# Kernel optimization log

Measured on AMD Instinct MI355X. Metric: run time of the kernel, lower is better.

The kernel has to match this reference:

```python
import jax, jax.numpy as jnp
import numpy as np

NB, NL, V, VOCAB, D, TOPK = 16, 64, 16384, 32000, 256, 16
NITER, EARLY, RW = 8, 2, 0.8


def setup_inputs():
    key = jax.random.key(0)
    ks = jax.random.split(key, 8)
    probas = jax.random.uniform(ks[0], (NB, NL, V), dtype=jnp.float32) + 1e-6
    h_d = jax.random.normal(ks[1], (NB, NL, D), dtype=jnp.float32)
    lengths = jax.random.randint(ks[2], (NB,), NL // 2, NL + 1)
    mask = (jnp.arange(NL)[None, :] < lengths[:, None]).astype(jnp.int32)  # prefix mask
    batch_vocab = jax.random.randint(ks[3], (V,), 0, VOCAB)
    emb_table = jax.random.normal(ks[4], (VOCAB, D), dtype=jnp.float32) * 0.02
    W1 = jax.random.normal(ks[5], (2 * D, D), dtype=jnp.float32) * 0.006
    b1 = jnp.zeros((D,), dtype=jnp.float32)
    return {"probas": probas, "h_d": h_d, "mask": mask, "batch_vocab": batch_vocab,
            "emb_table": emb_table, "W1": W1, "b1": b1}


def _forward(probas, h_d, mask, batch_vocab, emb_table, W1, b1):
    maskf = mask.astype(probas.dtype)
    MAP = jnp.argmax(probas, axis=-1)                       # [nb,nl]
    topk_vals, topk_idx = jax.lax.top_k(probas, TOPK)       # [nb,nl,K]
    topk_vals = jnp.where(mask[..., None] < 1, 1.0, topk_vals)
    logits = jnp.log(topk_vals)                             # Categorical(probs) == categorical(log p)
    sLens = jnp.sum(mask, axis=1)                           # [nb]
    one_hot = jnp.arange(NL)[None, :] == (sLens - 1)[:, None]  # one_hot_by_mask: last valid pos
    m2d = (mask[:, :, None] * mask[:, None, :]) > 0
    eyeM = jnp.eye(NL, dtype=probas.dtype)
    h_masked = h_d * maskf[..., None]

    def step(carry, k):
        max_score, best, count, stopped = carry
        choice = jax.random.categorical(k, logits)          # [nb,nl]
        samples = jnp.take_along_axis(topk_idx, choice[..., None], axis=-1)[..., 0]
        samples = jnp.where(one_hot, MAP, samples)
        embs = emb_table[batch_vocab[samples]] * maskf[..., None]   # gather+embed, masked
        new_embs = jax.nn.relu(jnp.concatenate([embs, h_masked], axis=-1) @ W1 + b1)
        Kmat = jnp.einsum('bld,bmd->blm', new_embs, new_embs)       # [nb,nl,nl]
        # det of leading lxl submatrix == det with padded rows/cols replaced by identity
        score = jnp.linalg.det(jnp.where(m2d, Kmat, eyeM))          # [nb]
        improved = score > max_score
        any_imp = jnp.any(improved)
        count = jnp.where(any_imp, 0, count + 1)
        upd = improved & (~stopped)
        stopped = stopped | ((~any_imp) & (count >= EARLY))
        max_score = jnp.where(upd, score, max_score)
        best = jnp.where(upd[:, None], samples, best)
        return (max_score, best, count, stopped), None

    init = (jnp.full((NB,), -jnp.inf, probas.dtype), MAP, jnp.int32(0), jnp.bool_(False))
    keys = jax.random.split(jax.random.key(42), NITER)
    (max_score, best, _, _), _ = jax.lax.scan(step, init, keys)

    # diverse_proba: scatter redist_weight at best choice, (1-rw) elsewhere, renormalize
    am = jnp.where(jnp.arange(V)[None, None, :] == best[:, :, None], RW, 1.0 - RW).astype(probas.dtype)
    x = probas * am
    nm = jnp.sum(x, axis=-1, keepdims=True)
    nm = jnp.where(maskf[..., None] == 0, 1e-10, nm)
    return x / nm, max_score


def reference(probas, h_d, mask, batch_vocab, emb_table, W1, b1):
    return _forward(probas, h_d, mask, batch_vocab, emb_table, W1, b1)
```

## Files before the change

kernel.cpp:

```cpp
#include <hip/hip_runtime.h>
#include <math.h>
#include <stdint.h>


#define TINYF 1.17549435082228750797e-38f

#define KMX(r, c) (((r) * 68) + ((c) ^ ((((r) >> 3) & 7) << 2)))

struct Keys16 { uint32_t k[16]; };

__host__ __device__ inline void tf2x32(uint32_t k0, uint32_t k1,
                                       uint32_t x0, uint32_t x1,
                                       uint32_t* o0, uint32_t* o1) {
  uint32_t ks2 = k0 ^ k1 ^ 0x1BD11BDAu;
  uint32_t ks[3] = {k0, k1, ks2};
  uint32_t v0 = x0 + k0, v1 = x1 + k1;
  const int R0[4] = {13, 15, 26, 6};
  const int R1[4] = {17, 29, 16, 24};
#pragma unroll
  for (int g = 0; g < 5; ++g) {
    const int* RR = (g & 1) ? R1 : R0;
#pragma unroll
    for (int r = 0; r < 4; ++r) {
      v0 += v1;
      v1 = (v1 << RR[r]) | (v1 >> (32 - RR[r]));
      v1 ^= v0;
    }
    v0 += ks[(g + 1) % 3];
    v1 += ks[(g + 2) % 3] + (uint32_t)(g + 1);
  }
  *o0 = v0; *o1 = v1;
}

__device__ inline float logf_ref(float x) { return (float)log((double)x); }

__device__ inline unsigned long long u64max(unsigned long long a,
                                            unsigned long long b) {
  return (a > b) ? a : b;
}

__device__ inline float lane_bcast_f32(float v, int slane) {
  return __uint_as_float(
      (unsigned)__builtin_amdgcn_readlane(__float_as_int(v), slane));
}

__global__ __launch_bounds__(256) void k_topk(const float* __restrict__ probas,
                                              const int* __restrict__ mask,
                                              int* __restrict__ topk_idx,
                                              float* __restrict__ logits,
                                              float* __restrict__ S) {
  int row = blockIdx.x;
  int t = threadIdx.x;
  const float* p = probas + (size_t)row * 16384;
  __shared__ unsigned long long lists[256][16];
  __shared__ float swsum[4];
  __shared__ int lcnt;
  unsigned long long* cand = &lists[0][0];

  cand[t] = 0ull;
  cand[t + 256] = 0ull;
  if (t == 0) lcnt = 0;
  __syncthreads();

  const uint32_t TB = 0x3F7E0000u;
  float sum = 0.f;
  const float4* p4 = (const float4*)p;
#pragma unroll 4
  for (int j = 0; j < 16; ++j) {
    float4 x = p4[t + j * 256];
    int v0 = (t + j * 256) * 4;
    uint32_t u0 = __float_as_uint(x.x), u1 = __float_as_uint(x.y);
    uint32_t u2 = __float_as_uint(x.z), u3 = __float_as_uint(x.w);
    sum += x.x; sum += x.y; sum += x.z; sum += x.w;
    uint32_t um = max(max(u0, u1), max(u2, u3));
    if (um >= TB) {
      if (u0 >= TB) { int s = atomicAdd(&lcnt, 1); if (s < 512)
          cand[s] = ((unsigned long long)u0 << 32) | (unsigned)(~(v0 + 0)); }
      if (u1 >= TB) { int s = atomicAdd(&lcnt, 1); if (s < 512)
          cand[s] = ((unsigned long long)u1 << 32) | (unsigned)(~(v0 + 1)); }
      if (u2 >= TB) { int s = atomicAdd(&lcnt, 1); if (s < 512)
          cand[s] = ((unsigned long long)u2 << 32) | (unsigned)(~(v0 + 2)); }
      if (u3 >= TB) { int s = atomicAdd(&lcnt, 1); if (s < 512)
          cand[s] = ((unsigned long long)u3 << 32) | (unsigned)(~(v0 + 3)); }
    }
  }
#pragma unroll
  for (int off = 32; off >= 1; off >>= 1) sum += __shfl_down(sum, off);
  if ((t & 63) == 0) swsum[t >> 6] = sum;
  __syncthreads();
  if (t == 0) S[row] = ((swsum[0] + swsum[1]) + swsum[2]) + swsum[3];

  int n = lcnt;
  if (n >= 16 && n <= 512) {
    if (t < 64) {
      unsigned long long c[8];
#pragma unroll
      for (int k = 0; k < 8; ++k) c[k] = cand[t + 64 * k];
      unsigned long long win = 0ull;
#pragma unroll
      for (int r = 0; r < 16; ++r) {
        unsigned long long m = c[0];
#pragma unroll
        for (int k = 1; k < 8; ++k) m = u64max(m, c[k]);
#pragma unroll
        for (int off = 32; off >= 1; off >>= 1) {
          unsigned long long o = __shfl_xor(m, off);
          m = u64max(m, o);
        }
        if (t == r) win = m;
#pragma unroll
        for (int k = 0; k < 8; ++k) if (c[k] == m) c[k] = 0ull;
      }
      if (t < 16) {
        int idx = (int)(~(unsigned)(win & 0xFFFFFFFFull));
        float val = __uint_as_float((unsigned)(win >> 32));
        topk_idx[row * 16 + t] = idx;
        logits[row * 16 + t] = (mask[row] == 0) ? 0.0f : logf_ref(val);
      }
    }
    return;
  }

  {
    unsigned long long loc[16];
#pragma unroll
    for (int q = 0; q < 16; ++q) loc[q] = 0ull;
    for (int j = 0; j < 64; ++j) {
      int v = t + j * 256;
      float x = p[v];
      unsigned long long key =
          ((unsigned long long)__float_as_uint(x) << 32) | (unsigned)(~v);
      if (key > loc[15]) {
        loc[15] = key;
#pragma unroll
        for (int q = 15; q > 0; --q) {
          if (loc[q] > loc[q - 1]) {
            unsigned long long tmp = loc[q]; loc[q] = loc[q - 1]; loc[q - 1] = tmp;
          }
        }
      }
    }
    __syncthreads();
#pragma unroll
    for (int q = 0; q < 16; ++q) lists[t][q] = loc[q];
    __syncthreads();
    for (int nl = 128; nl >= 1; nl >>= 1) {
      if (t < nl) {
        unsigned long long M[16];
        int ia = 0, ib = 0;
#pragma unroll
        for (int q = 0; q < 16; ++q) {
          unsigned long long av = lists[t][ia];
          unsigned long long bv = lists[t + nl][ib];
          if (av >= bv) { M[q] = av; ia++; } else { M[q] = bv; ib++; }
        }
#pragma unroll
        for (int q = 0; q < 16; ++q) lists[t][q] = M[q];
      }
      __syncthreads();
    }
    if (t < 16) {
      unsigned long long key = lists[0][t];
      int idx = (int)(~(unsigned)(key & 0xFFFFFFFFull));
      float val = __uint_as_float((unsigned)(key >> 32));
      topk_idx[row * 16 + t] = idx;
      logits[row * 16 + t] = (mask[row] == 0) ? 0.0f : logf_ref(val);
    }
  }
}

__global__ __launch_bounds__(256) void k_sample(Keys16 keys,
                                                const int* __restrict__ mask,
                                                const int* __restrict__ topk_idx,
                                                const float* __restrict__ logits,
                                                int* __restrict__ samples,
                                                int* __restrict__ choice) {
  int tid = blockIdx.x * 256 + threadIdx.x;
  int i = tid >> 10;
  int rbl = tid & 1023;
  int b = rbl >> 6;
  int l = rbl & 63;
  uint32_t k0 = keys.k[2 * i], k1 = keys.k[2 * i + 1];
  int sl = 0;
  for (int m = 0; m < 64; ++m) sl += mask[b * 64 + m];
  float bestv = 0.f; int bestk = 0;
#pragma unroll
  for (int k = 0; k < 16; ++k) {
    uint32_t j = (uint32_t)((b * 64 + l) * 16 + k);
    uint32_t y0, y1;
    tf2x32(k0, k1, 0u, j, &y0, &y1);
    uint32_t bits = y0 ^ y1;
    float f = __uint_as_float((bits >> 9) | 0x3f800000u) - 1.0f;
    float u = fmaxf(TINYF, f * 1.0f + TINYF);
    float t1 = logf_ref(u);
    float g = -logf_ref(-t1);
    float sv = g + logits[rbl * 16 + k];
    if (k == 0 || sv > bestv) { bestv = sv; bestk = k; }
  }
  int ce = (l == sl - 1) ? 0 : bestk;
  choice[tid] = ce;
  samples[tid] = topk_idx[rbl * 16 + ce];
}

__global__ __launch_bounds__(256) void k_ce(const int* __restrict__ topk_idx,
                                            const int* __restrict__ batch_vocab,
                                            const float* __restrict__ emb,
                                            const float* __restrict__ W1,
                                            const float* __restrict__ h_d,
                                            const float* __restrict__ b1,
                                            const int* __restrict__ mask,
                                            const int* __restrict__ choice,
                                            float* __restrict__ Eall) {
  int row = blockIdx.x;
  int t = threadIdx.x;
  __shared__ int smb;
  __shared__ int rid[8];
  __shared__ float e[8][256];
  __shared__ float hl[256];
  if (t == 0) smb = 0;
  float mkf = (float)mask[row];
  hl[t] = h_d[(size_t)row * 256 + t] * mkf;
  __syncthreads();
  if (t < 8) atomicOr(&smb, 1 << choice[t * 1024 + row]);
  __syncthreads();
  int mb = smb;
  if (t < 8) {
    int cnt = __popc(mb);
    int ss = (t < cnt) ? t : 0;
    int kk = 0;
    for (int bit = 0; bit < 16; ++bit) {
      if ((mb >> bit) & 1) {
        if (ss == 0) { kk = bit; break; }
        ss--;
      }
    }
    rid[t] = batch_vocab[topk_idx[row * 16 + kk]];
  }
  __syncthreads();
#pragma unroll
  for (int k = 0; k < 8; ++k) e[k][t] = emb[(size_t)rid[k] * 256 + t];
  __syncthreads();
  float acch = 0.f;
  for (int j0 = 0; j0 < 256; j0 += 4) {
    float4 hv = *(const float4*)&hl[j0];
    float w0 = W1[(256 + j0 + 0) * 256 + t];
    float w1 = W1[(256 + j0 + 1) * 256 + t];
    float w2 = W1[(256 + j0 + 2) * 256 + t];
    float w3 = W1[(256 + j0 + 3) * 256 + t];
    acch = fmaf(hv.x, w0, acch);
    acch = fmaf(hv.y, w1, acch);
    acch = fmaf(hv.z, w2, acch);
    acch = fmaf(hv.w, w3, acch);
  }
  float acc[8];
#pragma unroll
  for (int k = 0; k < 8; ++k) acc[k] = 0.f;
  for (int j0 = 0; j0 < 256; j0 += 4) {
    float w0 = W1[(j0 + 0) * 256 + t];
    float w1 = W1[(j0 + 1) * 256 + t];
    float w2 = W1[(j0 + 2) * 256 + t];
    float w3 = W1[(j0 + 3) * 256 + t];
#pragma unroll
    for (int k = 0; k < 8; ++k) {
      float4 ev = *(const float4*)&e[k][j0];
      acc[k] = fmaf(ev.x, w0, acc[k]);
      acc[k] = fmaf(ev.y, w1, acc[k]);
      acc[k] = fmaf(ev.z, w2, acc[k]);
      acc[k] = fmaf(ev.w, w3, acc[k]);
    }
  }
  float b1v = b1[t];
#pragma unroll
  for (int k = 0; k < 8; ++k) {
    float val = fmaf(mkf, acc[k], acch) + b1v;
    Eall[((size_t)row * 8 + k) * 256 + t] = fmaxf(val, 0.0f);
  }
}

__global__ __launch_bounds__(256, 1) void k_gram(const float* __restrict__ Eall,
                                                 const int* __restrict__ mask,
                                                 const int* __restrict__ choice,
                                                 float* __restrict__ scores) {
  int blk = blockIdx.x;
  int i = blk >> 4, b = blk & 15;
  int t = threadIdx.x;
  __shared__ __align__(16) float Ett[64][68];
  __shared__ __align__(16) float KmF[64 * 68];
  __shared__ int ch[64];
  int mskv = 0;
  if (t < 64) {
    int rowi = b * 64 + t;
    int ml = 0;
#pragma unroll
    for (int ii = 0; ii < 8; ++ii) ml |= 1 << choice[ii * 1024 + rowi];
    int cc = choice[i * 1024 + rowi];
    ch[t] = __popc(ml & ((1 << cc) - 1));
    mskv = mask[rowi];
  }
  __syncthreads();
  int l = t & 63, wd = t >> 6;
  const float* eptr =
      Eall + ((size_t)((b * 64 + l) * 8 + ch[l])) * 256 + wd * 16;
  float acc[16];
#pragma unroll
  for (int q = 0; q < 16; ++q) acc[q] = 0.f;
  int tx = t & 15, ty = t >> 4;
  for (int dt = 0; dt < 4; ++dt) {
    const float* src = eptr + dt * 64;
    float4 v0 = *(const float4*)(src + 0);
    float4 v1 = *(const float4*)(src + 4);
    float4 v2 = *(const float4*)(src + 8);
    float4 v3 = *(const float4*)(src + 12);
    int d0 = wd * 16;
    Ett[d0 +  0][l] = v0.x; Ett[d0 +  1][l] = v0.y;
    Ett[d0 +  2][l] = v0.z; Ett[d0 +  3][l] = v0.w;
    Ett[d0 +  4][l] = v1.x; Ett[d0 +  5][l] = v1.y;
    Ett[d0 +  6][l] = v1.z; Ett[d0 +  7][l] = v1.w;
    Ett[d0 +  8][l] = v2.x; Ett[d0 +  9][l] = v2.y;
    Ett[d0 + 10][l] = v2.z; Ett[d0 + 11][l] = v2.w;
    Ett[d0 + 12][l] = v3.x; Ett[d0 + 13][l] = v3.y;
    Ett[d0 + 14][l] = v3.z; Ett[d0 + 15][l] = v3.w;
    __syncthreads();
#pragma unroll 4
    for (int dd = 0; dd < 64; ++dd) {
      float4 av4 = *(const float4*)&Ett[dd][tx * 4];
      float4 bv4 = *(const float4*)&Ett[dd][ty * 4];
      float avv[4] = {av4.x, av4.y, av4.z, av4.w};
      float bvv[4] = {bv4.x, bv4.y, bv4.z, bv4.w};
#pragma unroll
      for (int a2 = 0; a2 < 4; ++a2)
#pragma unroll
        for (int c2 = 0; c2 < 4; ++c2)
          acc[a2 * 4 + c2] = fmaf(avv[a2], bvv[c2], acc[a2 * 4 + c2]);
    }
    __syncthreads();
  }
#pragma unroll
  for (int a2 = 0; a2 < 4; ++a2)
#pragma unroll
    for (int c2 = 0; c2 < 4; ++c2)
      KmF[KMX(tx * 4 + a2, ty * 4 + c2)] = acc[a2 * 4 + c2];
  __syncthreads();
  if (t >= 64) return;

  unsigned long long bal = __ballot(mskv != 0);
  int L = __popcll(bal);

#define KM_DECL(i) float4 r##i = *(const float4*)&KmF[KMX(t, 4 * i)];
  KM_DECL(0)  KM_DECL(1)  KM_DECL(2)  KM_DECL(3)
  KM_DECL(4)  KM_DECL(5)  KM_DECL(6)  KM_DECL(7)
  KM_DECL(8)  KM_DECL(9)  KM_DECL(10) KM_DECL(11)
  KM_DECL(12) KM_DECL(13) KM_DECL(14) KM_DECL(15)
#undef KM_DECL

  float sdet = 1.f, ssign = 1.f;
  int pos = t;
  float curcol = r0.x;

#pragma unroll 1
  for (int p = 0; p < L; ++p) {
    bool cnd = (pos >= p) && (pos < L);
    unsigned lo = (((unsigned)(63 - pos)) << 6) | (unsigned)t;
    unsigned long long key =
        cnd ? ((((unsigned long long)__float_as_uint(fabsf(curcol))) << 32) | lo)
            : 0ull;
#pragma unroll
    for (int off = 32; off >= 1; off >>= 1) {
      unsigned long long o = __shfl_xor(key, off);
      if (o > key) key = o;
    }
    int lane_rb = (int)(key & 63u);
    int pb = 63 - (int)((key >> 6) & 63u);
    int srb = __builtin_amdgcn_readfirstlane(lane_rb);
    float kpp = lane_bcast_f32(curcol, srb);
    sdet *= kpp;
    if (pb != p) ssign = -ssign;
    int np = pos;
    if (pos == p) np = pb;
    if (t == lane_rb) np = p;
    pos = np;
    bool active = (pos > p) && (pos < L);
    float f = (active && kpp != 0.f) ? (curcol / kpp) : 0.f;
    float nf = -f;
    int pp1 = p + 1;
#define KM_ELIM(i)                                                        \
    if (4 * i + 3 >= pp1) {                                               \
      float px = lane_bcast_f32(r##i.x, srb);                             \
      float py = lane_bcast_f32(r##i.y, srb);                             \
      float pz = lane_bcast_f32(r##i.z, srb);                             \
      float pw = lane_bcast_f32(r##i.w, srb);                             \
      r##i.x = fmaf(nf, px, r##i.x);                                      \
      r##i.y = fmaf(nf, py, r##i.y);                                      \
      r##i.z = fmaf(nf, pz, r##i.z);                                      \
      r##i.w = fmaf(nf, pw, r##i.w);                                      \
      if ((pp1 >> 2) == i) {    \
        int sel = pp1 & 3;                                                \
        curcol = (sel == 0) ? r##i.x : (sel == 1) ? r##i.y                \
               : (sel == 2) ? r##i.z : r##i.w;                            \
      }                                                                   \
    }
    KM_ELIM(0)  KM_ELIM(1)  KM_ELIM(2)  KM_ELIM(3)
    KM_ELIM(4)  KM_ELIM(5)  KM_ELIM(6)  KM_ELIM(7)
    KM_ELIM(8)  KM_ELIM(9)  KM_ELIM(10) KM_ELIM(11)
    KM_ELIM(12) KM_ELIM(13) KM_ELIM(14) KM_ELIM(15)
#undef KM_ELIM
  }
  if (t == 0) scores[i * 16 + b] = sdet * ssign;
}

__global__ __launch_bounds__(256) void k_out(const float* __restrict__ probas,
                                             const int* __restrict__ mask,
                                             const int* __restrict__ samples,
                                             const int* __restrict__ topk_idx,
                                             const float* __restrict__ scores,
                                             const float* __restrict__ S,
                                             float* __restrict__ out,
                                             float* __restrict__ out_ms) {
  int row = blockIdx.x;
  int b = row >> 6;
  int t = threadIdx.x;
  __shared__ float ssc[128];
  if (t < 128) ssc[t] = scores[t];
  __syncthreads();
  float ms[16]; int w[16];
#pragma unroll
  for (int q = 0; q < 16; ++q) { ms[q] = -INFINITY; w[q] = -1; }
  int count = 0; bool stopped = false;
#pragma unroll
  for (int i = 0; i < 8; ++i) {
    bool any = false; bool imp[16];
#pragma unroll
    for (int q = 0; q < 16; ++q) {
      imp[q] = ssc[i * 16 + q] > ms[q];
      any = any || imp[q];
    }
    count = any ? 0 : (count + 1);
#pragma unroll
    for (int q = 0; q < 16; ++q) {
      if (imp[q] && !stopped) { ms[q] = ssc[i * 16 + q]; w[q] = i; }
    }
    stopped = stopped || ((!any) && (count >= 2));
  }
  if (row == 0 && t == 0) {
#pragma unroll
    for (int q = 0; q < 16; ++q) out_ms[q] = ms[q];
  }
  int wi = -1;
#pragma unroll
  for (int q = 0; q < 16; ++q) if (b == q) wi = w[q];

  int best = (wi >= 0) ? samples[wi * 1024 + row] : topk_idx[row * 16];
  const float* p = probas + (size_t)row * 16384;
  float* o = out + (size_t)row * 16384;
  float nm;
  if (mask[row] == 0) {
    nm = 1e-10f;
  } else {
    nm = 0.2f * S[row] + 0.6f * p[best];
  }
  const float4* p4 = (const float4*)p;
  float4* o4 = (float4*)o;
  for (int f = t; f < 4096; f += 256) {
    float4 x = p4[f];
    int v0 = f << 2;
    float4 r;
    r.x = x.x * ((v0 + 0 == best) ? 0.8f : 0.2f) / nm;
    r.y = x.y * ((v0 + 1 == best) ? 0.8f : 0.2f) / nm;
    r.z = x.z * ((v0 + 2 == best) ? 0.8f : 0.2f) / nm;
    r.w = x.w * ((v0 + 3 == best) ? 0.8f : 0.2f) / nm;
    o4[f] = r;
  }
}

extern "C" void kernel_launch(void* const* d_in, const int* in_sizes, int n_in,
                              void* d_out, int out_size, void* d_ws, size_t ws_size,
                              hipStream_t stream) {
  const float* probas = (const float*)d_in[0];
  const float* h_d    = (const float*)d_in[1];
  const int*   mask   = (const int*)d_in[2];
  const int*   bvoc   = (const int*)d_in[3];
  const float* emb    = (const float*)d_in[4];
  const float* W1     = (const float*)d_in[5];
  const float* b1     = (const float*)d_in[6];
  float* out = (float*)d_out;

  char* w = (char*)d_ws;
  int*   topk_idx = (int*)w;   w += 16384 * sizeof(int);
  float* logits   = (float*)w; w += 16384 * sizeof(float);
  float* S        = (float*)w; w += 1024 * sizeof(float);
  int*   samples  = (int*)w;   w += 8192 * sizeof(int);
  int*   choice   = (int*)w;   w += 8192 * sizeof(int);
  float* scores   = (float*)w; w += 128 * sizeof(float);

  float* Eall = out;

  Keys16 keys;
  for (uint32_t i = 0; i < 8; ++i) {
    uint32_t a, bq;
    tf2x32(0u, 42u, 0u, i, &a, &bq);
    keys.k[2 * i] = a; keys.k[2 * i + 1] = bq;
  }

  k_topk<<<1024, 256, 0, stream>>>(probas, mask, topk_idx, logits, S);
  k_sample<<<32, 256, 0, stream>>>(keys, mask, topk_idx, logits, samples, choice);
  k_ce<<<1024, 256, 0, stream>>>(topk_idx, bvoc, emb, W1, h_d, b1, mask, choice,
                                 Eall);
  k_gram<<<128, 256, 0, stream>>>(Eall, mask, choice, scores);
  k_out<<<1024, 256, 0, stream>>>(probas, mask, samples, topk_idx, scores, S,
                                  out, out + 16777216);
}
```

Measured before the change: 281.7 us.

## Pipeline pivot search one column ahead and use DPP max reduction

Replaces the shuffle-based 64-bit argmax butterfly in the determinant's partial-pivoting loop with a DPP row/bcast reduction, reading the result from lane 63. It also computes the next column's eliminated values first, so the pivot search for step p+1 runs before the full row elimination of step p. This takes the cross-lane reduction off the critical dependency chain. The cost is extra register state and more complex bookkeeping for the lookahead column.

```diff
diff --git a/kernel.cpp b/kernel.cpp
--- a/kernel.cpp
+++ b/kernel.cpp
@@ -42,6 +42,26 @@
 __device__ inline float lane_bcast_f32(float v, int slane) {
   return __uint_as_float(
       (unsigned)__builtin_amdgcn_readlane(__float_as_int(v), slane));
+}
+
+template <int CTRL, int RMASK>
+__device__ inline void dpp_max_step(unsigned& hi, unsigned& lo) {
+  unsigned nh = (unsigned)__builtin_amdgcn_update_dpp(
+      0, (int)hi, CTRL, RMASK, 0xF, false);
+  unsigned nl = (unsigned)__builtin_amdgcn_update_dpp(
+      0, (int)lo, CTRL, RMASK, 0xF, false);
+  bool take = (nh > hi) || (nh == hi && nl > lo);
+  hi = take ? nh : hi;
+  lo = take ? nl : lo;
+}
+
+__device__ inline void dpp_reduce_max64(unsigned& hi, unsigned& lo) {
+  dpp_max_step<0x111, 0xF>(hi, lo);
+  dpp_max_step<0x112, 0xF>(hi, lo);
+  dpp_max_step<0x114, 0xF>(hi, lo);
+  dpp_max_step<0x118, 0xF>(hi, lo);
+  dpp_max_step<0x142, 0xA>(hi, lo);
+  dpp_max_step<0x143, 0xC>(hi, lo);
 }
 
 __global__ __launch_bounds__(256) void k_topk(const float* __restrict__ probas,
@@ -356,33 +376,41 @@
   float sdet = 1.f, ssign = 1.f;
   int pos = t;
   float curcol = r0.x;
+  float nextcol = r0.y;
+
+  unsigned khi, klo;
+  {
+    bool cnd = (pos < L);
+    khi = cnd ? __float_as_uint(fabsf(curcol)) : 0u;
+    klo = cnd ? ((((unsigned)(63 - pos)) << 6) | (unsigned)t) : 0u;
+    dpp_reduce_max64(khi, klo);
+  }
 
 #pragma unroll 1
   for (int p = 0; p < L; ++p) {
-    bool cnd = (pos >= p) && (pos < L);
-    unsigned lo = (((unsigned)(63 - pos)) << 6) | (unsigned)t;
-    unsigned long long key =
-        cnd ? ((((unsigned long long)__float_as_uint(fabsf(curcol))) << 32) | lo)
-            : 0ull;
-#pragma unroll
-    for (int off = 32; off >= 1; off >>= 1) {
-      unsigned long long o = __shfl_xor(key, off);
-      if (o > key) key = o;
-    }
-    int lane_rb = (int)(key & 63u);
-    int pb = 63 - (int)((key >> 6) & 63u);
-    int srb = __builtin_amdgcn_readfirstlane(lane_rb);
+    unsigned lo63 = (unsigned)__builtin_amdgcn_readlane((int)klo, 63);
+    int srb = (int)(lo63 & 63u);
+    int pb = 63 - (int)((lo63 >> 6) & 63u);
     float kpp = lane_bcast_f32(curcol, srb);
     sdet *= kpp;
     if (pb != p) ssign = -ssign;
     int np = pos;
     if (pos == p) np = pb;
-    if (t == lane_rb) np = p;
+    if (t == srb) np = p;
     pos = np;
     bool active = (pos > p) && (pos < L);
     float f = (active && kpp != 0.f) ? (curcol / kpp) : 0.f;
     float nf = -f;
-    int pp1 = p + 1;
+    float prn = lane_bcast_f32(nextcol, srb);
+    float nc1 = fmaf(nf, prn, nextcol);
+    int pp1 = p + 1, pp2 = p + 2;
+    {
+      bool cndn = (pos >= pp1) && (pos < L);
+      khi = cndn ? __float_as_uint(fabsf(nc1)) : 0u;
+      klo = cndn ? ((((unsigned)(63 - pos)) << 6) | (unsigned)t) : 0u;
+      dpp_reduce_max64(khi, klo);
+    }
+    float cap = nc1;
 #define KM_ELIM(i)                                                        \
     if (4 * i + 3 >= pp1) {                                               \
       float px = lane_bcast_f32(r##i.x, srb);                             \
@@ -393,10 +421,10 @@
       r##i.y = fmaf(nf, py, r##i.y);                                      \
       r##i.z = fmaf(nf, pz, r##i.z);                                      \
       r##i.w = fmaf(nf, pw, r##i.w);                                      \
-      if ((pp1 >> 2) == i) {    \
-        int sel = pp1 & 3;                                                \
-        curcol = (sel == 0) ? r##i.x : (sel == 1) ? r##i.y                \
-               : (sel == 2) ? r##i.z : r##i.w;                            \
+      if ((pp2 >> 2) == i) {          \
+        int sel = pp2 & 3;                                                \
+        cap = (sel == 0) ? r##i.x : (sel == 1) ? r##i.y                   \
+            : (sel == 2) ? r##i.z : r##i.w;                               \
       }                                                                   \
     }
     KM_ELIM(0)  KM_ELIM(1)  KM_ELIM(2)  KM_ELIM(3)
@@ -404,6 +432,8 @@
     KM_ELIM(8)  KM_ELIM(9)  KM_ELIM(10) KM_ELIM(11)
     KM_ELIM(12) KM_ELIM(13) KM_ELIM(14) KM_ELIM(15)
 #undef KM_ELIM
+    curcol = nc1;
+    nextcol = cap;
   }
   if (t == 0) scores[i * 16 + b] = sdet * ssign;
 }
```

New measurement: 277.0 us. Within noise of the previous version (-1.7%).
